# Kernel optimization log

Measured on AMD Instinct MI355X. Metric: run time of the kernel, lower is better.

Reference implementation:

```python
import jax, jax.numpy as jnp
import numpy as np

B, L, D = 64, 2048, 1024

def setup_inputs() -> dict:
    key = jax.random.key(0)
    k1, k2, k3 = jax.random.split(key, 3)
    seq = jax.random.normal(k1, (B, L, D), dtype=jnp.float32)
    begin = jax.random.randint(k2, (B,), 0, L // 2, dtype=jnp.int64)
    span = jax.random.randint(k3, (B,), 1, L // 2, dtype=jnp.int64)
    end = begin + span  # guaranteed begin < end <= L
    return {"seq": seq, "begin": begin, "end": end}

def reference(seq, begin, end):
    # Ragged segment mean: mean(seq[i, begin[i]:end[i]]) per sample.
    pos = jnp.arange(seq.shape[1])  # [L]
    mask = (pos[None, :] >= begin[:, None]) & (pos[None, :] < end[:, None])  # [B, L]
    m = mask.astype(seq.dtype)
    ssum = jnp.einsum('bl,bld->bd', m, seq)  # masked sum over seq dim
    count = (end - begin).astype(seq.dtype)[:, None]  # [B, 1]
    return ssum / count
```

## Files before the change

kernel.cpp:

```cpp
#include <hip/hip_runtime.h>

#define B_ 64
#define L_ 2048
#define D_ 1024
#define SPLIT 64

__global__ __launch_bounds__(256) void seg_mean_stage1(
    const float* __restrict__ seq,
    const int* __restrict__ begin,
    const int* __restrict__ end,
    float* __restrict__ ws)
{
    const int s  = blockIdx.x;
    const int b  = blockIdx.y;
    const int bg = begin[b];
    const int en = end[b];
    const int len = en - bg;

    const int per = (len + SPLIT - 1) / SPLIT;
    const int l0  = bg + s * per;
    const int l1  = min(l0 + per, en);

    const int col = threadIdx.x;
    const float4* __restrict__ base =
        reinterpret_cast<const float4*>(seq + (size_t)b * L_ * D_);

    float4 a0 = make_float4(0.f, 0.f, 0.f, 0.f);
    float4 a1 = a0, a2 = a0, a3 = a0;

    int l = l0;
    for (; l + 4 <= l1; l += 4) {
        float4 v0 = base[(size_t)(l + 0) * (D_ / 4) + col];
        float4 v1 = base[(size_t)(l + 1) * (D_ / 4) + col];
        float4 v2 = base[(size_t)(l + 2) * (D_ / 4) + col];
        float4 v3 = base[(size_t)(l + 3) * (D_ / 4) + col];
        a0.x += v0.x; a0.y += v0.y; a0.z += v0.z; a0.w += v0.w;
        a1.x += v1.x; a1.y += v1.y; a1.z += v1.z; a1.w += v1.w;
        a2.x += v2.x; a2.y += v2.y; a2.z += v2.z; a2.w += v2.w;
        a3.x += v3.x; a3.y += v3.y; a3.z += v3.z; a3.w += v3.w;
    }
    for (; l < l1; ++l) {
        float4 v = base[(size_t)l * (D_ / 4) + col];
        a0.x += v.x; a0.y += v.y; a0.z += v.z; a0.w += v.w;
    }

    const float inv = 1.0f / (float)len;
    float4 t;
    t.x = (a0.x + a1.x + a2.x + a3.x) * inv;
    t.y = (a0.y + a1.y + a2.y + a3.y) * inv;
    t.z = (a0.z + a1.z + a2.z + a3.z) * inv;
    t.w = (a0.w + a1.w + a2.w + a3.w) * inv;

    float4* __restrict__ w4 = reinterpret_cast<float4*>(ws);
    w4[((size_t)(b * SPLIT + s)) * (D_ / 4) + col] = t;
}

__global__ __launch_bounds__(256) void seg_mean_stage2(
    const float* __restrict__ ws,
    float* __restrict__ out)
{
    const int b   = blockIdx.x;
    const int col = threadIdx.x;
    const float4* __restrict__ w4 =
        reinterpret_cast<const float4*>(ws) + (size_t)b * SPLIT * (D_ / 4);

    float4 acc = make_float4(0.f, 0.f, 0.f, 0.f);
    #pragma unroll
    for (int s = 0; s < SPLIT; ++s) {
        float4 v = w4[(size_t)s * (D_ / 4) + col];
        acc.x += v.x; acc.y += v.y; acc.z += v.z; acc.w += v.w;
    }
    reinterpret_cast<float4*>(out)[(size_t)b * (D_ / 4) + col] = acc;
}

extern "C" void kernel_launch(void* const* d_in, const int* in_sizes, int n_in,
                              void* d_out, int out_size, void* d_ws, size_t ws_size,
                              hipStream_t stream) {
    const float* seq   = (const float*)d_in[0];
    const int*   begin = (const int*)d_in[1];
    const int*   end   = (const int*)d_in[2];
    float*       out   = (float*)d_out;
    float*       ws    = (float*)d_ws;

    dim3 g1(SPLIT, B_);
    seg_mean_stage1<<<g1, 256, 0, stream>>>(seq, begin, end, ws);
    seg_mean_stage2<<<B_, 256, 0, stream>>>(ws, out);
}
```

Before: 32.76 us.

## Skip empty split blocks and parallelize stage-2 reduction across splits

Stage 1 blocks with an empty row range now exit early without writing partials. Stage 2 reads only the number of split chunks that actually hold data, and spreads the reduction over four columns-by-four split-groups per block with a shared-memory combine, which gives four times as many blocks. This cuts wasted partial traffic and raises stage-2 parallelism, at the cost of an extra barrier and reading begin/end again.

```diff
diff --git a/kernel.cpp b/kernel.cpp
--- a/kernel.cpp
+++ b/kernel.cpp
@@ -20,6 +20,7 @@
     const int per = (len + SPLIT - 1) / SPLIT;
     const int l0  = bg + s * per;
     const int l1  = min(l0 + per, en);
+    if (l0 >= l1) return;
 
     const int col = threadIdx.x;
     const float4* __restrict__ base =
@@ -57,20 +58,45 @@
 
 __global__ __launch_bounds__(256) void seg_mean_stage2(
     const float* __restrict__ ws,
+    const int* __restrict__ begin,
+    const int* __restrict__ end,
     float* __restrict__ out)
 {
-    const int b   = blockIdx.x;
-    const int col = threadIdx.x;
+    const int b    = blockIdx.x;
+    const int q    = blockIdx.y;
+    const int lane = threadIdx.x & 63;
+    const int sg   = threadIdx.x >> 6;
+    const int col4 = q * 64 + lane;
+
+    const int len = end[b] - begin[b];
+    const int per = (len + SPLIT - 1) / SPLIT;
+    const int ns  = (len + per - 1) / per;
+
     const float4* __restrict__ w4 =
         reinterpret_cast<const float4*>(ws) + (size_t)b * SPLIT * (D_ / 4);
 
     float4 acc = make_float4(0.f, 0.f, 0.f, 0.f);
-    #pragma unroll
-    for (int s = 0; s < SPLIT; ++s) {
-        float4 v = w4[(size_t)s * (D_ / 4) + col];
+    for (int s = sg; s < ns; s += 4) {
+        float4 v = w4[(size_t)s * (D_ / 4) + col4];
         acc.x += v.x; acc.y += v.y; acc.z += v.z; acc.w += v.w;
     }
-    reinterpret_cast<float4*>(out)[(size_t)b * (D_ / 4) + col] = acc;
+
+    __shared__ float4 red[256];
+    red[threadIdx.x] = acc;
+    __syncthreads();
+
+    if (sg == 0) {
+        float4 r0 = red[lane];
+        float4 r1 = red[lane + 64];
+        float4 r2 = red[lane + 128];
+        float4 r3 = red[lane + 192];
+        float4 t;
+        t.x = (r0.x + r1.x) + (r2.x + r3.x);
+        t.y = (r0.y + r1.y) + (r2.y + r3.y);
+        t.z = (r0.z + r1.z) + (r2.z + r3.z);
+        t.w = (r0.w + r1.w) + (r2.w + r3.w);
+        reinterpret_cast<float4*>(out)[(size_t)b * (D_ / 4) + col4] = t;
+    }
 }
 
 extern "C" void kernel_launch(void* const* d_in, const int* in_sizes, int n_in,
@@ -84,5 +110,6 @@
 
     dim3 g1(SPLIT, B_);
     seg_mean_stage1<<<g1, 256, 0, stream>>>(seq, begin, end, ws);
-    seg_mean_stage2<<<B_, 256, 0, stream>>>(ws, out);
+    dim3 g2(B_, 4);
+    seg_mean_stage2<<<g2, 256, 0, stream>>>(ws, begin, end, out);
 }
```

Result: slower. 35.35 us (+7.9%).

## Split by column groups with LDS row reduction and fp16 workspace

Applied to the files above, without the earlier changes.

Stage 1 now gives each block a 32-column slice of one half of the segment. Its 256 threads each stride over rows, and the per-thread partials are combined in shared memory. This cuts the partial-sum workspace from 64 splits to 2 per batch, and the partials are stored as fp16, which removes most of the workspace write/read traffic. Stage 2 becomes a simple elementwise sum of two halves. In exchange, each wavefront reads only 128-byte row pieces instead of full rows, which may hurt DRAM coalescing, and fp16 intermediates lose precision.

```diff
diff --git a/kernel.cpp b/kernel.cpp
--- a/kernel.cpp
+++ b/kernel.cpp
@@ -1,76 +1,100 @@
 #include <hip/hip_runtime.h>
+#include <hip/hip_fp16.h>
 
 #define B_ 64
 #define L_ 2048
 #define D_ 1024
-#define SPLIT 64
+#define D4 (D_ / 4)
+#define CG 32
+#define RS 2
 
 __global__ __launch_bounds__(256) void seg_mean_stage1(
     const float* __restrict__ seq,
     const int* __restrict__ begin,
     const int* __restrict__ end,
-    float* __restrict__ ws)
+    __half* __restrict__ ws)
 {
-    const int s  = blockIdx.x;
+    const int gc = blockIdx.x;
+    const int g  = gc >> 1;
+    const int r  = gc & 1;
     const int b  = blockIdx.y;
-    const int bg = begin[b];
-    const int en = end[b];
+
+    const int bg  = begin[b];
+    const int en  = end[b];
     const int len = en - bg;
+    const int half = (len + 1) >> 1;
+    const int l0 = (r == 0) ? bg : bg + half;
+    const int l1 = (r == 0) ? bg + half : en;
 
-    const int per = (len + SPLIT - 1) / SPLIT;
-    const int l0  = bg + s * per;
-    const int l1  = min(l0 + per, en);
+    const int col8   = threadIdx.x & 7;
+    const int rowoff = threadIdx.x >> 3;
 
-    const int col = threadIdx.x;
     const float4* __restrict__ base =
-        reinterpret_cast<const float4*>(seq + (size_t)b * L_ * D_);
+        reinterpret_cast<const float4*>(seq) + (size_t)b * (L_ * D4) + g * 8 + col8;
 
     float4 a0 = make_float4(0.f, 0.f, 0.f, 0.f);
     float4 a1 = a0, a2 = a0, a3 = a0;
 
-    int l = l0;
-    for (; l + 4 <= l1; l += 4) {
-        float4 v0 = base[(size_t)(l + 0) * (D_ / 4) + col];
-        float4 v1 = base[(size_t)(l + 1) * (D_ / 4) + col];
-        float4 v2 = base[(size_t)(l + 2) * (D_ / 4) + col];
-        float4 v3 = base[(size_t)(l + 3) * (D_ / 4) + col];
+    int l = l0 + rowoff;
+    for (; l < l1 - 96; l += 128) {
+        float4 v0 = base[(size_t)(l +  0) * D4];
+        float4 v1 = base[(size_t)(l + 32) * D4];
+        float4 v2 = base[(size_t)(l + 64) * D4];
+        float4 v3 = base[(size_t)(l + 96) * D4];
         a0.x += v0.x; a0.y += v0.y; a0.z += v0.z; a0.w += v0.w;
         a1.x += v1.x; a1.y += v1.y; a1.z += v1.z; a1.w += v1.w;
         a2.x += v2.x; a2.y += v2.y; a2.z += v2.z; a2.w += v2.w;
         a3.x += v3.x; a3.y += v3.y; a3.z += v3.z; a3.w += v3.w;
     }
-    for (; l < l1; ++l) {
-        float4 v = base[(size_t)l * (D_ / 4) + col];
+    for (; l < l1; l += 32) {
+        float4 v = base[(size_t)l * D4];
         a0.x += v.x; a0.y += v.y; a0.z += v.z; a0.w += v.w;
     }
 
-    const float inv = 1.0f / (float)len;
-    float4 t;
-    t.x = (a0.x + a1.x + a2.x + a3.x) * inv;
-    t.y = (a0.y + a1.y + a2.y + a3.y) * inv;
-    t.z = (a0.z + a1.z + a2.z + a3.z) * inv;
-    t.w = (a0.w + a1.w + a2.w + a3.w) * inv;
+    float4 acc;
+    acc.x = (a0.x + a1.x) + (a2.x + a3.x);
+    acc.y = (a0.y + a1.y) + (a2.y + a3.y);
+    acc.z = (a0.z + a1.z) + (a2.z + a3.z);
+    acc.w = (a0.w + a1.w) + (a2.w + a3.w);
 
-    float4* __restrict__ w4 = reinterpret_cast<float4*>(ws);
-    w4[((size_t)(b * SPLIT + s)) * (D_ / 4) + col] = t;
+    __shared__ float4 red[256];
+    red[threadIdx.x] = acc;
+    __syncthreads();
+    #pragma unroll
+    for (int s = 128; s >= 8; s >>= 1) {
+        if (threadIdx.x < s) {
+            float4 o = red[threadIdx.x + s];
+            red[threadIdx.x].x += o.x;
+            red[threadIdx.x].y += o.y;
+            red[threadIdx.x].z += o.z;
+            red[threadIdx.x].w += o.w;
+        }
+        __syncthreads();
+    }
+
+    if (threadIdx.x < 8) {
+        float4 t = red[threadIdx.x];
+        const float inv = 1.0f / (float)len;
+        union { __half2 h2[2]; float2 f2; } u;
+        u.h2[0] = __floats2half2_rn(t.x * inv, t.y * inv);
+        u.h2[1] = __floats2half2_rn(t.z * inv, t.w * inv);
+        float2* __restrict__ w2 = reinterpret_cast<float2*>(ws);
+        w2[(size_t)(((b * CG + g) * RS + r)) * 8 + threadIdx.x] = u.f2;
+    }
 }
 
 __global__ __launch_bounds__(256) void seg_mean_stage2(
-    const float* __restrict__ ws,
+    const __half* __restrict__ ws,
     float* __restrict__ out)
 {
-    const int b   = blockIdx.x;
-    const int col = threadIdx.x;
-    const float4* __restrict__ w4 =
-        reinterpret_cast<const float4*>(ws) + (size_t)b * SPLIT * (D_ / 4);
+    const int idx = blockIdx.x * 256 + threadIdx.x;
+    const int b   = idx >> 10;
+    const int col = idx & 1023;
+    const int g   = col >> 5;
+    const int c   = col & 31;
 
-    float4 acc = make_float4(0.f, 0.f, 0.f, 0.f);
-    #pragma unroll
-    for (int s = 0; s < SPLIT; ++s) {
-        float4 v = w4[(size_t)s * (D_ / 4) + col];
-        acc.x += v.x; acc.y += v.y; acc.z += v.z; acc.w += v.w;
-    }
-    reinterpret_cast<float4*>(out)[(size_t)b * (D_ / 4) + col] = acc;
+    const size_t s0 = (size_t)((b * CG + g) * RS) * 32 + c;
+    out[idx] = __half2float(ws[s0]) + __half2float(ws[s0 + 32]);
 }
 
 extern "C" void kernel_launch(void* const* d_in, const int* in_sizes, int n_in,
@@ -80,9 +104,9 @@
     const int*   begin = (const int*)d_in[1];
     const int*   end   = (const int*)d_in[2];
     float*       out   = (float*)d_out;
-    float*       ws    = (float*)d_ws;
+    __half*      ws    = (__half*)d_ws;
 
-    dim3 g1(SPLIT, B_);
+    dim3 g1(CG * RS, B_);
     seg_mean_stage1<<<g1, 256, 0, stream>>>(seq, begin, end, ws);
-    seg_mean_stage2<<<B_, 256, 0, stream>>>(ws, out);
+    seg_mean_stage2<<<B_ * D_ / 65536 * 256, 256, 0, stream>>>(ws, out);
 }
```

Measured after the change: 30.17 us. 7.9% less time.
